# Kernel tuning notes

Hardware: AMD Instinct MI355X
Metric: run time of the kernel (lower is better)

The kernel has to match this reference:

```python
import math
import jax, jax.numpy as jnp
import numpy as np

B, S, E, H = 4, 2048, 1024, 16
HD = E // H  # 64


def setup_inputs() -> dict:
    key = jax.random.key(0)
    ks = jax.random.split(key, 7)
    scale = 1.0 / math.sqrt(E)
    return {
        "x": jax.random.normal(ks[0], (B, S, E), dtype=jnp.float32),
        "Wq": jax.random.normal(ks[1], (H, HD, E), dtype=jnp.float32) * scale,
        "bq": jax.random.normal(ks[2], (H, HD), dtype=jnp.float32) * 0.01,
        "Wk": jax.random.normal(ks[3], (H, HD, E), dtype=jnp.float32) * scale,
        "bk": jax.random.normal(ks[4], (H, HD), dtype=jnp.float32) * 0.01,
        "Wv": jax.random.normal(ks[5], (H, HD, E), dtype=jnp.float32) * scale,
        "bv": jax.random.normal(ks[6], (H, HD), dtype=jnp.float32) * 0.01,
    }


def reference(x, Wq, bq, Wk, bk, Wv, bv):
    b, s, e = x.shape
    h, hd, _ = Wq.shape
    inv_scale = 1.0 / math.sqrt(hd)
    # per-head linear projections (torch Linear: x @ W^T + b), batched over heads
    q = jnp.einsum("bse,hde->bshd", x, Wq) + bq  # [B,S,H,HD]
    k = jnp.einsum("bse,hde->bshd", x, Wk) + bk
    v = jnp.einsum("bse,hde->bshd", x, Wv) + bv
    # causal mask: -inf above diagonal (added before scaling, as in source;
    # -inf * inv_scale is still -inf so math is identical)
    mask = jnp.triu(jnp.full((s, s), -jnp.inf, dtype=x.dtype), k=1)
    scores = (jnp.einsum("bqhd,bkhd->bhqk", q, k) + mask) * inv_scale  # [B,H,S,S]
    attn = jax.nn.softmax(scores, axis=-1)
    out = jnp.einsum("bhqk,bkhd->bqhd", attn, v)  # [B,S,H,HD]
    # concat over heads in head order == reshape with head-major last dims
    return out.reshape(b, s, h * hd)
```

## Files before the change

### kernel.cpp

```cpp
#include <hip/hip_runtime.h>


typedef __bf16 bf16x8 __attribute__((ext_vector_type(8)));
typedef __bf16 bf16x4 __attribute__((ext_vector_type(4)));
typedef float f32x4 __attribute__((ext_vector_type(4)));
typedef unsigned short us8 __attribute__((ext_vector_type(8)));
typedef unsigned short us4 __attribute__((ext_vector_type(4)));

#define Bb 4
#define Ss 2048
#define Ee 1024
#define Hh 16
#define HD 64

#if __has_builtin(__builtin_amdgcn_exp2f)
#define EXP2(x) __builtin_amdgcn_exp2f(x)
#else
#define EXP2(x) exp2f(x)
#endif

__device__ __forceinline__ unsigned short f2bf(float f) {
  union { float f; unsigned u; } v; v.f = f;
  unsigned u = v.u;
  u += 0x7fffu + ((u >> 16) & 1u);
  return (unsigned short)(u >> 16);
}

__device__ __forceinline__ void gl_lds16(const void* g, void* l) {
  __builtin_amdgcn_global_load_lds((const __attribute__((address_space(1))) void*)g,
                                   (__attribute__((address_space(3))) void*)l, 16, 0, 0);
}

#define DSR(d, a, o) asm volatile("ds_read_b128 %0, %1 offset:" #o : "=v"(d) : "v"(a))

__global__ __launch_bounds__(256) void cvt_all(const float* __restrict__ x,
                                               const float* __restrict__ wq,
                                               const float* __restrict__ wk,
                                               const float* __restrict__ wv,
                                               unsigned short* __restrict__ xb,
                                               unsigned short* __restrict__ wb) {
  int i = blockIdx.x * 256 + threadIdx.x;
  const float* src; unsigned short* dst; int idx;
  if (i < 2097152)      { src = x;  dst = xb;                idx = i; }
  else if (i < 2359296) { src = wq; dst = wb;                idx = i - 2097152; }
  else if (i < 2621440) { src = wk; dst = wb + 1048576;      idx = i - 2359296; }
  else                  { src = wv; dst = wb + 2 * 1048576;  idx = i - 2621440; }
  float4 f = ((const float4*)src)[idx];
  us4 o = { f2bf(f.x), f2bf(f.y), f2bf(f.z), f2bf(f.w) };
  ((us4*)dst)[idx] = o;
}

__global__ __launch_bounds__(256, 2) void qkv_gemm(const unsigned short* __restrict__ xb,
                                                   const unsigned short* __restrict__ wb_all,
                                                   const float* __restrict__ bq,
                                                   const float* __restrict__ bk,
                                                   const float* __restrict__ bv,
                                                   unsigned short* __restrict__ qkv) {
  const int z = blockIdx.z;
  const unsigned short* wb = wb_all + (size_t)z * (Ee * Ee);
  const float* bias = (z == 0) ? bq : (z == 1) ? bk : bv;
  unsigned short* outb = qkv + (size_t)z * (Bb * Ss * Ee);
  const float osc = (z == 0) ? 0.180336880f : 1.0f;

  __shared__ unsigned short SMEM[32768];

  const int t = threadIdx.x;
  const int wave = t >> 6, lane = t & 63, quad = lane >> 4, ln = lane & 15;
  const int wr = wave >> 1, wc = wave & 1;
  const int m0 = blockIdx.x * 128, n0 = blockIdx.y * 128;

  const int r32 = t >> 3;
  const int cs = ((t & 7) ^ (r32 & 7)) * 8;
  const int t8 = t * 8;
  const unsigned short* gA0 = xb + (size_t)(m0 + r32) * Ee + cs;
  const unsigned short* gA1 = gA0 + 64 * Ee;
  const unsigned short* gB0 = wb + (size_t)(n0 + r32) * Ee + cs;
  const unsigned short* gB1 = gB0 + 64 * Ee;

  const int swz0 = ((0 * 4 + quad) ^ (ln & 7)) * 16;
  const int swz1 = ((1 * 4 + quad) ^ (ln & 7)) * 16;
  int aA0 = (wr * 32 + ln) * 128 + swz0;
  int aA1 = (wr * 32 + ln) * 128 + swz1;
  int bA0 = 16384 + (wc * 32 + ln) * 128 + swz0;
  int bA1 = 16384 + (wc * 32 + ln) * 128 + swz1;

  f32x4 acc[2][2][2][2] = {};
  bf16x8 af[2][2], bf0[2][2], bf1[2][2];

  gl_lds16(gA0,           &SMEM[t8]);
  gl_lds16(gA0 + 32 * Ee, &SMEM[t8 + 2048]);
  gl_lds16(gB0,           &SMEM[8192 + t8]);
  gl_lds16(gB0 + 32 * Ee, &SMEM[8192 + t8 + 2048]);
  gl_lds16(gB1,           &SMEM[12288 + t8]);
  gl_lds16(gB1 + 32 * Ee, &SMEM[12288 + t8 + 2048]);
  gl_lds16(gA1,           &SMEM[4096 + t8]);
  gl_lds16(gA1 + 32 * Ee, &SMEM[4096 + t8 + 2048]);

#pragma unroll 1
  for (int kt = 0; kt < 15; ++kt) {
    const int sbuf = ((kt & 1) << 14) ^ 16384;
    const int co = (kt + 1) * 64;

    asm volatile("s_waitcnt vmcnt(4)" ::: "memory");
    asm volatile("s_barrier" ::: "memory");
    DSR(af[0][0], aA0, 0);    DSR(af[1][0], aA0, 2048);
    DSR(af[0][1], aA1, 0);    DSR(af[1][1], aA1, 2048);
    DSR(bf0[0][0], bA0, 0);   DSR(bf0[1][0], bA0, 2048);
    DSR(bf0[0][1], bA1, 0);   DSR(bf0[1][1], bA1, 2048);
    gl_lds16(gA0 + co,           &SMEM[sbuf + t8]);
    gl_lds16(gA0 + co + 32 * Ee, &SMEM[sbuf + t8 + 2048]);
    asm volatile("s_barrier" ::: "memory");
    asm volatile("s_waitcnt lgkmcnt(0)" ::: "memory");
    __builtin_amdgcn_sched_barrier(0);
    __builtin_amdgcn_s_setprio(1);
#pragma unroll
    for (int kk = 0; kk < 2; ++kk)
#pragma unroll
      for (int i = 0; i < 2; ++i)
#pragma unroll
        for (int j = 0; j < 2; ++j)
          acc[0][0][i][j] = __builtin_amdgcn_mfma_f32_16x16x32_bf16(af[i][kk], bf0[j][kk], acc[0][0][i][j], 0, 0, 0);
    __builtin_amdgcn_s_setprio(0);
    __builtin_amdgcn_sched_barrier(0);

    asm volatile("s_waitcnt vmcnt(4)" ::: "memory");
    asm volatile("s_barrier" ::: "memory");
    DSR(bf1[0][0], bA0, 8192); DSR(bf1[1][0], bA0, 10240);
    DSR(bf1[0][1], bA1, 8192); DSR(bf1[1][1], bA1, 10240);
    gl_lds16(gB0 + co,           &SMEM[sbuf + 8192 + t8]);
    gl_lds16(gB0 + co + 32 * Ee, &SMEM[sbuf + 8192 + t8 + 2048]);
    asm volatile("s_barrier" ::: "memory");
    asm volatile("s_waitcnt lgkmcnt(0)" ::: "memory");
    __builtin_amdgcn_sched_barrier(0);
    __builtin_amdgcn_s_setprio(1);
#pragma unroll
    for (int kk = 0; kk < 2; ++kk)
#pragma unroll
      for (int i = 0; i < 2; ++i)
#pragma unroll
        for (int j = 0; j < 2; ++j)
          acc[0][1][i][j] = __builtin_amdgcn_mfma_f32_16x16x32_bf16(af[i][kk], bf1[j][kk], acc[0][1][i][j], 0, 0, 0);
    __builtin_amdgcn_s_setprio(0);
    __builtin_amdgcn_sched_barrier(0);

    asm volatile("s_waitcnt vmcnt(4)" ::: "memory");
    asm volatile("s_barrier" ::: "memory");
    DSR(af[0][0], aA0, 8192); DSR(af[1][0], aA0, 10240);
    DSR(af[0][1], aA1, 8192); DSR(af[1][1], aA1, 10240);
    gl_lds16(gB1 + co,           &SMEM[sbuf + 12288 + t8]);
    gl_lds16(gB1 + co + 32 * Ee, &SMEM[sbuf + 12288 + t8 + 2048]);
    asm volatile("s_barrier" ::: "memory");
    asm volatile("s_waitcnt lgkmcnt(0)" ::: "memory");
    __builtin_amdgcn_sched_barrier(0);
    __builtin_amdgcn_s_setprio(1);
#pragma unroll
    for (int kk = 0; kk < 2; ++kk)
#pragma unroll
      for (int i = 0; i < 2; ++i)
#pragma unroll
        for (int j = 0; j < 2; ++j)
          acc[1][0][i][j] = __builtin_amdgcn_mfma_f32_16x16x32_bf16(af[i][kk], bf0[j][kk], acc[1][0][i][j], 0, 0, 0);
    __builtin_amdgcn_s_setprio(0);
    __builtin_amdgcn_sched_barrier(0);

    asm volatile("s_barrier" ::: "memory");
    gl_lds16(gA1 + co,           &SMEM[sbuf + 4096 + t8]);
    gl_lds16(gA1 + co + 32 * Ee, &SMEM[sbuf + 4096 + t8 + 2048]);
    asm volatile("s_barrier" ::: "memory");
    __builtin_amdgcn_sched_barrier(0);
    __builtin_amdgcn_s_setprio(1);
#pragma unroll
    for (int kk = 0; kk < 2; ++kk)
#pragma unroll
      for (int i = 0; i < 2; ++i)
#pragma unroll
        for (int j = 0; j < 2; ++j)
          acc[1][1][i][j] = __builtin_amdgcn_mfma_f32_16x16x32_bf16(af[i][kk], bf1[j][kk], acc[1][1][i][j], 0, 0, 0);
    __builtin_amdgcn_s_setprio(0);
    __builtin_amdgcn_sched_barrier(0);

    aA0 ^= 32768; aA1 ^= 32768; bA0 ^= 32768; bA1 ^= 32768;
  }

  {
    asm volatile("s_waitcnt vmcnt(0)" ::: "memory");
    asm volatile("s_barrier" ::: "memory");
    DSR(af[0][0], aA0, 0);    DSR(af[1][0], aA0, 2048);
    DSR(af[0][1], aA1, 0);    DSR(af[1][1], aA1, 2048);
    DSR(bf0[0][0], bA0, 0);   DSR(bf0[1][0], bA0, 2048);
    DSR(bf0[0][1], bA1, 0);   DSR(bf0[1][1], bA1, 2048);
    DSR(bf1[0][0], bA0, 8192); DSR(bf1[1][0], bA0, 10240);
    DSR(bf1[0][1], bA1, 8192); DSR(bf1[1][1], bA1, 10240);
    asm volatile("s_waitcnt lgkmcnt(0)" ::: "memory");
    __builtin_amdgcn_sched_barrier(0);
#pragma unroll
    for (int kk = 0; kk < 2; ++kk)
#pragma unroll
      for (int i = 0; i < 2; ++i)
#pragma unroll
        for (int j = 0; j < 2; ++j) {
          acc[0][0][i][j] = __builtin_amdgcn_mfma_f32_16x16x32_bf16(af[i][kk], bf0[j][kk], acc[0][0][i][j], 0, 0, 0);
          acc[0][1][i][j] = __builtin_amdgcn_mfma_f32_16x16x32_bf16(af[i][kk], bf1[j][kk], acc[0][1][i][j], 0, 0, 0);
        }
    __builtin_amdgcn_sched_barrier(0);
    DSR(af[0][0], aA0, 8192); DSR(af[1][0], aA0, 10240);
    DSR(af[0][1], aA1, 8192); DSR(af[1][1], aA1, 10240);
    asm volatile("s_waitcnt lgkmcnt(0)" ::: "memory");
    __builtin_amdgcn_sched_barrier(0);
#pragma unroll
    for (int kk = 0; kk < 2; ++kk)
#pragma unroll
      for (int i = 0; i < 2; ++i)
#pragma unroll
        for (int j = 0; j < 2; ++j) {
          acc[1][0][i][j] = __builtin_amdgcn_mfma_f32_16x16x32_bf16(af[i][kk], bf0[j][kk], acc[1][0][i][j], 0, 0, 0);
          acc[1][1][i][j] = __builtin_amdgcn_mfma_f32_16x16x32_bf16(af[i][kk], bf1[j][kk], acc[1][1][i][j], 0, 0, 0);
        }
    __builtin_amdgcn_sched_barrier(0);
  }

  float biasj[2][2];
#pragma unroll
  for (int qb = 0; qb < 2; ++qb)
#pragma unroll
    for (int j = 0; j < 2; ++j)
      biasj[qb][j] = bias[n0 + qb * 64 + wc * 32 + j * 16 + ln];

  if (z != 2) {
#pragma unroll
    for (int qa = 0; qa < 2; ++qa)
#pragma unroll
      for (int qb = 0; qb < 2; ++qb)
#pragma unroll
        for (int i = 0; i < 2; ++i)
#pragma unroll
          for (int j = 0; j < 2; ++j)
#pragma unroll
            for (int r = 0; r < 4; ++r) {
              int m = m0 + qa * 64 + wr * 32 + i * 16 + quad * 4 + r;
              int n = n0 + qb * 64 + wc * 32 + j * 16 + ln;
              int b_ = m >> 11, s = m & 2047;
              int h = n >> 6, d = n & 63;
              outb[(((size_t)b_ * Hh + h) * Ss + s) * HD + d] =
                  f2bf((acc[qa][qb][i][j][r] + biasj[qb][j]) * osc);
            }
  } else {
    __syncthreads();
#pragma unroll
    for (int qa = 0; qa < 2; ++qa)
#pragma unroll
      for (int qb = 0; qb < 2; ++qb)
#pragma unroll
        for (int i = 0; i < 2; ++i)
#pragma unroll
          for (int j = 0; j < 2; ++j)
#pragma unroll
            for (int r = 0; r < 4; ++r) {
              int nc = qb * 64 + wc * 32 + j * 16 + ln;
              int mr = qa * 64 + wr * 32 + i * 16 + quad * 4 + r;
              SMEM[nc * 136 + mr] = f2bf(acc[qa][qb][i][j][r] + biasj[qb][j]);
            }
    __syncthreads();
    int nr = t >> 1, mh = t & 1;
    int n = n0 + nr, h = n >> 6, d = n & 63;
    int b_ = m0 >> 11;
    int s0 = (m0 & 2047) + mh * 64;
#pragma unroll
    for (int q = 0; q < 8; ++q) {
      us8 vdat = *(const us8*)&SMEM[nr * 136 + mh * 64 + q * 8];
      *(us8*)&outb[(((size_t)b_ * Hh + h) * HD + d) * Ss + s0 + q * 8] = vdat;
    }
  }
}

__global__ __launch_bounds__(512, 2) void flash_attn(const unsigned short* __restrict__ qkv,
                                                     float* __restrict__ out) {
  const int id = blockIdx.x;
  const int bh = id & 63;
  const int p = id >> 6;
  const int b_ = bh >> 4, h = bh & 15;

  const unsigned short* qb  = qkv + (size_t)bh * (Ss * HD);
  const unsigned short* kb  = qkv + (size_t)(64 + bh) * (Ss * HD);
  const unsigned short* vtb = qkv + (size_t)(128 + bh) * (Ss * HD);

  __shared__ __bf16 Ks[8192];
  __shared__ __bf16 Vt[8192];
  __shared__ __bf16 Ps[8][16][72];

  const int t = threadIdx.x;
  const int wave = t >> 6, lane = t & 63, quad = lane >> 4, ln = lane & 15;
  const int uw = wave >> 2;

  const int rk = t >> 3;
  const int ck = ((t & 7) ^ (rk & 7)) * 8;
  const int rv = t >> 4;
  const int cv = ((t & 15) ^ (rv & 7)) * 8;
  const int t8 = t * 8;

  const int qts[2] = { 15 - p, p };
  const int KTB = qts[0] + 1;
  const int su0 = 2 * qts[0] + uw;
  const int su1 = 2 * qts[1] + uw;
  const int qrow0 = qts[0] * 128 + wave * 16 + ln;
  const int qrow1 = qts[1] * 128 + wave * 16 + ln;

  bf16x8 qf[2][2];
#pragma unroll
  for (int qt = 0; qt < 2; ++qt)
#pragma unroll
    for (int ks = 0; ks < 2; ++ks)
      qf[qt][ks] = *(const bf16x8*)(qb + (size_t)(qts[qt] * 128 + wave * 16 + ln) * HD +
                                    ks * 32 + quad * 8);

  bf16x8 onef;
#pragma unroll
  for (int j = 0; j < 8; ++j) onef[j] = (__bf16)1.0f;

  f32x4 o[2][4] = {};
  f32x4 l4[2] = {};

#pragma unroll 1
  for (int kt = 0; kt < KTB; ++kt) {
    const unsigned short* kbt = kb + (size_t)kt * (128 * HD);
    const unsigned short* vbt = vtb + kt * 128;
    __syncthreads();
    gl_lds16(kbt + rk * HD + ck,        &Ks[t8]);
    gl_lds16(kbt + (rk + 64) * HD + ck, &Ks[t8 + 4096]);
    gl_lds16(vbt + rv * Ss + cv,        &Vt[t8]);
    gl_lds16(vbt + (rv + 32) * Ss + cv, &Vt[t8 + 4096]);
    __syncthreads();

#pragma unroll
    for (int h2 = 0; h2 < 2; ++h2) {
      const int kb64 = kt * 2 + h2;
      if (kb64 > su0) continue;
      const bool a1 = (kb64 <= su1);

      f32x4 s0[4] = {}, s1[4] = {};
#pragma unroll
      for (int g = 0; g < 4; ++g)
#pragma unroll
        for (int ks = 0; ks < 2; ++ks) {
          bf16x8 kf = *(const bf16x8*)&Ks[(h2 * 64 + g * 16 + ln) * 64 +
                                          (((ks * 4 + quad) ^ (ln & 7)) * 8)];
          s0[g] = __builtin_amdgcn_mfma_f32_16x16x32_bf16(kf, qf[0][ks], s0[g], 0, 0, 0);
          s1[g] = __builtin_amdgcn_mfma_f32_16x16x32_bf16(kf, qf[1][ks], s1[g], 0, 0, 0);
        }

      const int k0 = kb64 * 64;
      if (kb64 == su0) {
#pragma unroll
        for (int g = 0; g < 4; ++g)
#pragma unroll
          for (int r = 0; r < 4; ++r) {
            int kcol = k0 + g * 16 + quad * 4 + r;
            if (kcol > qrow0) s0[g][r] = -__builtin_inff();
          }
      }

#pragma unroll
      for (int g = 0; g < 4; ++g) {
        bf16x4 pk = { (__bf16)EXP2(s0[g][0]), (__bf16)EXP2(s0[g][1]),
                      (__bf16)EXP2(s0[g][2]), (__bf16)EXP2(s0[g][3]) };
        *(bf16x4*)&Ps[wave][ln][g * 16 + quad * 4] = pk;
      }
      bf16x8 pf0[2], pf1[2];
#pragma unroll
      for (int ks = 0; ks < 2; ++ks)
        pf0[ks] = *(const bf16x8*)&Ps[wave][ln][ks * 32 + quad * 8];

      if (a1) {
        if (kb64 == su1) {
#pragma unroll
          for (int g = 0; g < 4; ++g)
#pragma unroll
            for (int r = 0; r < 4; ++r) {
              int kcol = k0 + g * 16 + quad * 4 + r;
              if (kcol > qrow1) s1[g][r] = -__builtin_inff();
            }
        }
#pragma unroll
        for (int g = 0; g < 4; ++g) {
          bf16x4 pk = { (__bf16)EXP2(s1[g][0]), (__bf16)EXP2(s1[g][1]),
                        (__bf16)EXP2(s1[g][2]), (__bf16)EXP2(s1[g][3]) };
          *(bf16x4*)&Ps[wave][ln][g * 16 + quad * 4] = pk;
        }
#pragma unroll
        for (int ks = 0; ks < 2; ++ks)
          pf1[ks] = *(const bf16x8*)&Ps[wave][ln][ks * 32 + quad * 8];
      } else {
        pf1[0] = bf16x8{};
        pf1[1] = bf16x8{};
      }

      l4[0] = __builtin_amdgcn_mfma_f32_16x16x32_bf16(pf0[0], onef, l4[0], 0, 0, 0);
      l4[0] = __builtin_amdgcn_mfma_f32_16x16x32_bf16(pf0[1], onef, l4[0], 0, 0, 0);
      l4[1] = __builtin_amdgcn_mfma_f32_16x16x32_bf16(pf1[0], onef, l4[1], 0, 0, 0);
      l4[1] = __builtin_amdgcn_mfma_f32_16x16x32_bf16(pf1[1], onef, l4[1], 0, 0, 0);

#pragma unroll
      for (int g = 0; g < 4; ++g)
#pragma unroll
        for (int ks = 0; ks < 2; ++ks) {
          bf16x8 vf = *(const bf16x8*)&Vt[(g * 16 + ln) * 128 +
                                          (((h2 * 8 + ks * 4 + quad) ^ (ln & 7)) * 8)];
          o[0][g] = __builtin_amdgcn_mfma_f32_16x16x32_bf16(pf0[ks], vf, o[0][g], 0, 0, 0);
          o[1][g] = __builtin_amdgcn_mfma_f32_16x16x32_bf16(pf1[ks], vf, o[1][g], 0, 0, 0);
        }
    }
  }

#pragma unroll
  for (int qt = 0; qt < 2; ++qt) {
    float linv[4];
#pragma unroll
    for (int r = 0; r < 4; ++r) linv[r] = 1.0f / l4[qt][r];
#pragma unroll
    for (int g = 0; g < 4; ++g)
#pragma unroll
      for (int r = 0; r < 4; ++r) {
        int orow = qts[qt] * 128 + wave * 16 + quad * 4 + r;
        out[((size_t)b_ * Ss + orow) * Ee + h * HD + g * 16 + ln] = o[qt][g][r] * linv[r];
      }
  }
}

extern "C" void kernel_launch(void* const* d_in, const int* in_sizes, int n_in,
                              void* d_out, int out_size, void* d_ws, size_t ws_size,
                              hipStream_t stream) {
  const float* x  = (const float*)d_in[0];
  const float* Wq = (const float*)d_in[1];
  const float* bq = (const float*)d_in[2];
  const float* Wk = (const float*)d_in[3];
  const float* bk = (const float*)d_in[4];
  const float* Wv = (const float*)d_in[5];
  const float* bv = (const float*)d_in[6];
  float* out = (float*)d_out;

  unsigned short* ws  = (unsigned short*)d_ws;
  unsigned short* xb  = ws;
  unsigned short* wb  = ws + 8388608;
  unsigned short* qkv = ws + 8388608 + 3 * 1048576;

  cvt_all<<<11264, 256, 0, stream>>>(x, Wq, Wk, Wv, xb, wb);
  qkv_gemm<<<dim3(64, 8, 3), 256, 0, stream>>>(xb, wb, bq, bk, bv, qkv);
  flash_attn<<<512, 512, 0, stream>>>(qkv, out);
}
```

Measured before the change: 201.8 us.

## Double-buffer 64-key K/V tiles in LDS with async prefetch and inline-asm reads

Restructures the flash-attention loop to stage 64-key K and V tiles into a double-buffered LDS region. The next tile's global-to-LDS load is issued before computing the current one, replacing the two full-block syncthreads per 128-key tile with vmcnt waits and raw barriers. LDS reads and writes use inline ds_read_b128/ds_write_b64 with explicit lgkmcnt waits, and the second query tile's MFMAs are skipped when it is fully masked. The aim is to hide global load latency behind MFMA work. In exchange it adds more barrier iterations and hand-placed waits that can serialise LDS access.

Measured after the change: 199.9 us. About the same (-1.0%).

```diff
diff --git a/kernel.cpp b/kernel.cpp
--- a/kernel.cpp
+++ b/kernel.cpp
@@ -32,6 +32,8 @@
 }
 
 #define DSR(d, a, o) asm volatile("ds_read_b128 %0, %1 offset:" #o : "=v"(d) : "v"(a))
+#define DSW(a, d, o) asm volatile("ds_write_b64 %0, %1 offset:" #o :: "v"(a), "v"(d) : "memory")
+#define LGKM0 asm volatile("s_waitcnt lgkmcnt(0)" ::: "memory"); __builtin_amdgcn_sched_barrier(0)
 
 __global__ __launch_bounds__(256) void cvt_all(const float* __restrict__ x,
                                                const float* __restrict__ wq,
@@ -284,27 +286,28 @@
   const unsigned short* kb  = qkv + (size_t)(64 + bh) * (Ss * HD);
   const unsigned short* vtb = qkv + (size_t)(128 + bh) * (Ss * HD);
 
-  __shared__ __bf16 Ks[8192];
-  __shared__ __bf16 Vt[8192];
-  __shared__ __bf16 Ps[8][16][72];
+  __shared__ __bf16 LDS[25600];
 
   const int t = threadIdx.x;
   const int wave = t >> 6, lane = t & 63, quad = lane >> 4, ln = lane & 15;
   const int uw = wave >> 2;
 
-  const int rk = t >> 3;
-  const int ck = ((t & 7) ^ (rk & 7)) * 8;
-  const int rv = t >> 4;
-  const int cv = ((t & 15) ^ (rv & 7)) * 8;
+  const int r6 = t >> 3;
+  const int cstage = ((t & 7) ^ (r6 & 7)) * 8;
   const int t8 = t * 8;
 
   const int qts[2] = { 15 - p, p };
-  const int KTB = qts[0] + 1;
+  const int KTB = 2 * qts[0] + 2;
   const int su0 = 2 * qts[0] + uw;
   const int su1 = 2 * qts[1] + uw;
   const int qrow0 = qts[0] * 128 + wave * 16 + ln;
   const int qrow1 = qts[1] * 128 + wave * 16 + ln;
 
+  int ka0 = ln * 128 + ((quad ^ (ln & 7)) * 16);
+  int ka1 = ln * 128 + (((4 + quad) ^ (ln & 7)) * 16);
+  const int pw = (16384 + (wave * 16 + ln) * 72 + quad * 4) * 2;
+  const int pr = (16384 + (wave * 16 + ln) * 72 + quad * 8) * 2;
+
   bf16x8 qf[2][2];
 #pragma unroll
   for (int qt = 0; qt < 2; ++qt)
@@ -320,96 +323,143 @@
   f32x4 o[2][4] = {};
   f32x4 l4[2] = {};
 
-#pragma unroll 1
-  for (int kt = 0; kt < KTB; ++kt) {
-    const unsigned short* kbt = kb + (size_t)kt * (128 * HD);
-    const unsigned short* vbt = vtb + kt * 128;
-    __syncthreads();
-    gl_lds16(kbt + rk * HD + ck,        &Ks[t8]);
-    gl_lds16(kbt + (rk + 64) * HD + ck, &Ks[t8 + 4096]);
-    gl_lds16(vbt + rv * Ss + cv,        &Vt[t8]);
-    gl_lds16(vbt + (rv + 32) * Ss + cv, &Vt[t8 + 4096]);
-    __syncthreads();
-
-#pragma unroll
-    for (int h2 = 0; h2 < 2; ++h2) {
-      const int kb64 = kt * 2 + h2;
-      if (kb64 > su0) continue;
-      const bool a1 = (kb64 <= su1);
-
-      f32x4 s0[4] = {}, s1[4] = {};
+  auto body = [&](int kt) {
+    if (kt > su0) return;
+    const bool a1 = (kt <= su1);
+    const int k0 = kt * 64;
+    f32x4 s0[4] = {}, s1[4] = {};
+    bf16x8 kf[2][2];
+
+    DSR(kf[0][0], ka0, 0);    DSR(kf[1][0], ka0, 2048);
+    DSR(kf[0][1], ka1, 0);    DSR(kf[1][1], ka1, 2048);
+    LGKM0;
+#pragma unroll
+    for (int ks = 0; ks < 2; ++ks) {
+      s0[0] = __builtin_amdgcn_mfma_f32_16x16x32_bf16(kf[0][ks], qf[0][ks], s0[0], 0, 0, 0);
+      s0[1] = __builtin_amdgcn_mfma_f32_16x16x32_bf16(kf[1][ks], qf[0][ks], s0[1], 0, 0, 0);
+    }
+    if (a1)
+#pragma unroll
+      for (int ks = 0; ks < 2; ++ks) {
+        s1[0] = __builtin_amdgcn_mfma_f32_16x16x32_bf16(kf[0][ks], qf[1][ks], s1[0], 0, 0, 0);
+        s1[1] = __builtin_amdgcn_mfma_f32_16x16x32_bf16(kf[1][ks], qf[1][ks], s1[1], 0, 0, 0);
+      }
+    DSR(kf[0][0], ka0, 4096); DSR(kf[1][0], ka0, 6144);
+    DSR(kf[0][1], ka1, 4096); DSR(kf[1][1], ka1, 6144);
+    LGKM0;
+#pragma unroll
+    for (int ks = 0; ks < 2; ++ks) {
+      s0[2] = __builtin_amdgcn_mfma_f32_16x16x32_bf16(kf[0][ks], qf[0][ks], s0[2], 0, 0, 0);
+      s0[3] = __builtin_amdgcn_mfma_f32_16x16x32_bf16(kf[1][ks], qf[0][ks], s0[3], 0, 0, 0);
+    }
+    if (a1)
+#pragma unroll
+      for (int ks = 0; ks < 2; ++ks) {
+        s1[2] = __builtin_amdgcn_mfma_f32_16x16x32_bf16(kf[0][ks], qf[1][ks], s1[2], 0, 0, 0);
+        s1[3] = __builtin_amdgcn_mfma_f32_16x16x32_bf16(kf[1][ks], qf[1][ks], s1[3], 0, 0, 0);
+      }
+
+    if (kt == su0) {
 #pragma unroll
       for (int g = 0; g < 4; ++g)
 #pragma unroll
-        for (int ks = 0; ks < 2; ++ks) {
-          bf16x8 kf = *(const bf16x8*)&Ks[(h2 * 64 + g * 16 + ln) * 64 +
-                                          (((ks * 4 + quad) ^ (ln & 7)) * 8)];
-          s0[g] = __builtin_amdgcn_mfma_f32_16x16x32_bf16(kf, qf[0][ks], s0[g], 0, 0, 0);
-          s1[g] = __builtin_amdgcn_mfma_f32_16x16x32_bf16(kf, qf[1][ks], s1[g], 0, 0, 0);
+        for (int r = 0; r < 4; ++r) {
+          int kcol = k0 + g * 16 + quad * 4 + r;
+          if (kcol > qrow0) s0[g][r] = -__builtin_inff();
         }
-
-      const int k0 = kb64 * 64;
-      if (kb64 == su0) {
+    }
+    {
+      bf16x4 pk;
+      pk = bf16x4{ (__bf16)EXP2(s0[0][0]), (__bf16)EXP2(s0[0][1]), (__bf16)EXP2(s0[0][2]), (__bf16)EXP2(s0[0][3]) };
+      DSW(pw, pk, 0);
+      pk = bf16x4{ (__bf16)EXP2(s0[1][0]), (__bf16)EXP2(s0[1][1]), (__bf16)EXP2(s0[1][2]), (__bf16)EXP2(s0[1][3]) };
+      DSW(pw, pk, 32);
+      pk = bf16x4{ (__bf16)EXP2(s0[2][0]), (__bf16)EXP2(s0[2][1]), (__bf16)EXP2(s0[2][2]), (__bf16)EXP2(s0[2][3]) };
+      DSW(pw, pk, 64);
+      pk = bf16x4{ (__bf16)EXP2(s0[3][0]), (__bf16)EXP2(s0[3][1]), (__bf16)EXP2(s0[3][2]), (__bf16)EXP2(s0[3][3]) };
+      DSW(pw, pk, 96);
+    }
+    bf16x8 pf0[2], pf1[2];
+    DSR(pf0[0], pr, 0); DSR(pf0[1], pr, 64);
+    LGKM0;
+
+    if (a1) {
+      if (kt == su1) {
 #pragma unroll
         for (int g = 0; g < 4; ++g)
 #pragma unroll
           for (int r = 0; r < 4; ++r) {
             int kcol = k0 + g * 16 + quad * 4 + r;
-            if (kcol > qrow0) s0[g][r] = -__builtin_inff();
+            if (kcol > qrow1) s1[g][r] = -__builtin_inff();
           }
       }
-
-#pragma unroll
-      for (int g = 0; g < 4; ++g) {
-        bf16x4 pk = { (__bf16)EXP2(s0[g][0]), (__bf16)EXP2(s0[g][1]),
-                      (__bf16)EXP2(s0[g][2]), (__bf16)EXP2(s0[g][3]) };
-        *(bf16x4*)&Ps[wave][ln][g * 16 + quad * 4] = pk;
-      }
-      bf16x8 pf0[2], pf1[2];
-#pragma unroll
-      for (int ks = 0; ks < 2; ++ks)
-        pf0[ks] = *(const bf16x8*)&Ps[wave][ln][ks * 32 + quad * 8];
-
-      if (a1) {
-        if (kb64 == su1) {
-#pragma unroll
-          for (int g = 0; g < 4; ++g)
-#pragma unroll
-            for (int r = 0; r < 4; ++r) {
-              int kcol = k0 + g * 16 + quad * 4 + r;
-              if (kcol > qrow1) s1[g][r] = -__builtin_inff();
-            }
-        }
-#pragma unroll
-        for (int g = 0; g < 4; ++g) {
-          bf16x4 pk = { (__bf16)EXP2(s1[g][0]), (__bf16)EXP2(s1[g][1]),
-                        (__bf16)EXP2(s1[g][2]), (__bf16)EXP2(s1[g][3]) };
-          *(bf16x4*)&Ps[wave][ln][g * 16 + quad * 4] = pk;
-        }
-#pragma unroll
-        for (int ks = 0; ks < 2; ++ks)
-          pf1[ks] = *(const bf16x8*)&Ps[wave][ln][ks * 32 + quad * 8];
-      } else {
-        pf1[0] = bf16x8{};
-        pf1[1] = bf16x8{};
-      }
-
-      l4[0] = __builtin_amdgcn_mfma_f32_16x16x32_bf16(pf0[0], onef, l4[0], 0, 0, 0);
-      l4[0] = __builtin_amdgcn_mfma_f32_16x16x32_bf16(pf0[1], onef, l4[0], 0, 0, 0);
+      bf16x4 pk;
+      pk = bf16x4{ (__bf16)EXP2(s1[0][0]), (__bf16)EXP2(s1[0][1]), (__bf16)EXP2(s1[0][2]), (__bf16)EXP2(s1[0][3]) };
+      DSW(pw, pk, 0);
+      pk = bf16x4{ (__bf16)EXP2(s1[1][0]), (__bf16)EXP2(s1[1][1]), (__bf16)EXP2(s1[1][2]), (__bf16)EXP2(s1[1][3]) };
+      DSW(pw, pk, 32);
+      pk = bf16x4{ (__bf16)EXP2(s1[2][0]), (__bf16)EXP2(s1[2][1]), (__bf16)EXP2(s1[2][2]), (__bf16)EXP2(s1[2][3]) };
+      DSW(pw, pk, 64);
+      pk = bf16x4{ (__bf16)EXP2(s1[3][0]), (__bf16)EXP2(s1[3][1]), (__bf16)EXP2(s1[3][2]), (__bf16)EXP2(s1[3][3]) };
+      DSW(pw, pk, 96);
+      DSR(pf1[0], pr, 0); DSR(pf1[1], pr, 64);
+      LGKM0;
+    }
+
+    l4[0] = __builtin_amdgcn_mfma_f32_16x16x32_bf16(pf0[0], onef, l4[0], 0, 0, 0);
+    l4[0] = __builtin_amdgcn_mfma_f32_16x16x32_bf16(pf0[1], onef, l4[0], 0, 0, 0);
+    if (a1) {
       l4[1] = __builtin_amdgcn_mfma_f32_16x16x32_bf16(pf1[0], onef, l4[1], 0, 0, 0);
       l4[1] = __builtin_amdgcn_mfma_f32_16x16x32_bf16(pf1[1], onef, l4[1], 0, 0, 0);
-
-#pragma unroll
-      for (int g = 0; g < 4; ++g)
-#pragma unroll
-        for (int ks = 0; ks < 2; ++ks) {
-          bf16x8 vf = *(const bf16x8*)&Vt[(g * 16 + ln) * 128 +
-                                          (((h2 * 8 + ks * 4 + quad) ^ (ln & 7)) * 8)];
-          o[0][g] = __builtin_amdgcn_mfma_f32_16x16x32_bf16(pf0[ks], vf, o[0][g], 0, 0, 0);
-          o[1][g] = __builtin_amdgcn_mfma_f32_16x16x32_bf16(pf1[ks], vf, o[1][g], 0, 0, 0);
-        }
-    }
+    }
+
+    DSR(kf[0][0], ka0, 16384); DSR(kf[1][0], ka0, 18432);
+    DSR(kf[0][1], ka1, 16384); DSR(kf[1][1], ka1, 18432);
+    LGKM0;
+#pragma unroll
+    for (int ks = 0; ks < 2; ++ks) {
+      o[0][0] = __builtin_amdgcn_mfma_f32_16x16x32_bf16(pf0[ks], kf[0][ks], o[0][0], 0, 0, 0);
+      o[0][1] = __builtin_amdgcn_mfma_f32_16x16x32_bf16(pf0[ks], kf[1][ks], o[0][1], 0, 0, 0);
+    }
+    if (a1)
+#pragma unroll
+      for (int ks = 0; ks < 2; ++ks) {
+        o[1][0] = __builtin_amdgcn_mfma_f32_16x16x32_bf16(pf1[ks], kf[0][ks], o[1][0], 0, 0, 0);
+        o[1][1] = __builtin_amdgcn_mfma_f32_16x16x32_bf16(pf1[ks], kf[1][ks], o[1][1], 0, 0, 0);
+      }
+    DSR(kf[0][0], ka0, 20480); DSR(kf[1][0], ka0, 22528);
+    DSR(kf[0][1], ka1, 20480); DSR(kf[1][1], ka1, 22528);
+    LGKM0;
+#pragma unroll
+    for (int ks = 0; ks < 2; ++ks) {
+      o[0][2] = __builtin_amdgcn_mfma_f32_16x16x32_bf16(pf0[ks], kf[0][ks], o[0][2], 0, 0, 0);
+      o[0][3] = __builtin_amdgcn_mfma_f32_16x16x32_bf16(pf0[ks], kf[1][ks], o[0][3], 0, 0, 0);
+    }
+    if (a1)
+#pragma unroll
+      for (int ks = 0; ks < 2; ++ks) {
+        o[1][2] = __builtin_amdgcn_mfma_f32_16x16x32_bf16(pf1[ks], kf[0][ks], o[1][2], 0, 0, 0);
+        o[1][3] = __builtin_amdgcn_mfma_f32_16x16x32_bf16(pf1[ks], kf[1][ks], o[1][3], 0, 0, 0);
+      }
+  };
+
+  gl_lds16(kb + r6 * HD + cstage,  &LDS[t8]);
+  gl_lds16(vtb + r6 * Ss + cstage, &LDS[8192 + t8]);
+
+#pragma unroll 1
+  for (int kt = 0; kt < KTB - 1; ++kt) {
+    const int sb = (kt & 1) ^ 1;
+    gl_lds16(kb + (size_t)(kt + 1) * (64 * HD) + r6 * HD + cstage, &LDS[sb * 4096 + t8]);
+    gl_lds16(vtb + (kt + 1) * 64 + r6 * Ss + cstage,               &LDS[8192 + sb * 4096 + t8]);
+    asm volatile("s_waitcnt vmcnt(2)" ::: "memory");
+    asm volatile("s_barrier" ::: "memory");
+    body(kt);
+    asm volatile("s_barrier" ::: "memory");
+    ka0 ^= 8192; ka1 ^= 8192;
   }
+  asm volatile("s_waitcnt vmcnt(0)" ::: "memory");
+  asm volatile("s_barrier" ::: "memory");
+  body(KTB - 1);
 
 #pragma unroll
   for (int qt = 0; qt < 2; ++qt) {
```
